# Kernel optimization log

Hardware: AMD Instinct MI355X
Metric: run time of the kernel (lower is better)

Reference implementation:

```python
import jax, jax.numpy as jnp
import numpy as np

N_EMBD = 768
N_HEAD = 12
B, T = 4, 2048
EPS = 1e-5


def layernorm(x, w, b):
    mu = jnp.mean(x, axis=-1, keepdims=True)
    var = jnp.mean(jnp.square(x - mu), axis=-1, keepdims=True)
    return (x - mu) * jax.lax.rsqrt(var + EPS) * w + b


def setup_inputs() -> dict:
    key = jax.random.key(0)
    ks = jax.random.split(key, 6)
    C = N_EMBD
    s = 0.02
    return {
        "x": jax.random.normal(ks[0], (B, T, C), jnp.float32),
        "ln1_w": jnp.ones((C,), jnp.float32),
        "ln1_b": jnp.zeros((C,), jnp.float32),
        "W_qkv": jax.random.normal(ks[1], (C, 3 * C), jnp.float32) * s,
        "b_qkv": jnp.zeros((3 * C,), jnp.float32),
        "W_attnproj": jax.random.normal(ks[2], (C, C), jnp.float32) * s,
        "b_attnproj": jnp.zeros((C,), jnp.float32),
        "ln2_w": jnp.ones((C,), jnp.float32),
        "ln2_b": jnp.zeros((C,), jnp.float32),
        "W_fc": jax.random.normal(ks[3], (C, 4 * C), jnp.float32) * s,
        "b_fc": jnp.zeros((4 * C,), jnp.float32),
        "W_mlpproj": jax.random.normal(ks[4], (4 * C, C), jnp.float32) * s,
        "b_mlpproj": jnp.zeros((C,), jnp.float32),
    }


def reference(x, ln1_w, ln1_b, W_qkv, b_qkv, W_attnproj, b_attnproj,
              ln2_w, ln2_b, W_fc, b_fc, W_mlpproj, b_mlpproj):
    Bx, Tx, C = x.shape
    H = N_HEAD
    Dh = C // H

    # --- attention branch ---
    h = layernorm(x, ln1_w, ln1_b)
    qkv = h @ W_qkv + b_qkv                       # [B, T, 3C]
    q, k, v = jnp.split(qkv, 3, axis=-1)
    q = q.reshape(Bx, Tx, H, Dh).transpose(0, 2, 1, 3)  # [B, H, T, Dh]
    k = k.reshape(Bx, Tx, H, Dh).transpose(0, 2, 1, 3)
    v = v.reshape(Bx, Tx, H, Dh).transpose(0, 2, 1, 3)
    att = jnp.einsum('bhqd,bhkd->bhqk', q, k) * (1.0 / np.sqrt(Dh))
    att = jax.nn.softmax(att, axis=-1)            # full softmax attention (no mask)
    y = jnp.einsum('bhqk,bhkd->bhqd', att, v)     # [B, H, T, Dh]
    y = y.transpose(0, 2, 1, 3).reshape(Bx, Tx, C)
    y = y @ W_attnproj + b_attnproj
    x = x + y

    # --- MLP branch ---
    h = layernorm(x, ln2_w, ln2_b)
    h = jax.nn.gelu(h @ W_fc + b_fc, approximate=False)
    h = h @ W_mlpproj + b_mlpproj
    return x + h
```

## Files before the change

### kernel.cpp

```cpp
#include <hip/hip_runtime.h>

typedef __bf16 bf16x8 __attribute__((ext_vector_type(8)));
typedef __bf16 bf16x4 __attribute__((ext_vector_type(4)));
typedef float f32x4 __attribute__((ext_vector_type(4)));
typedef unsigned short u16;
typedef unsigned long long u64;

#define GL2LDS(gp, lp) __builtin_amdgcn_global_load_lds(                      \
    (const __attribute__((address_space(1))) void*)(gp),                      \
    (__attribute__((address_space(3))) void*)(lp), 16, 0, 0)

__device__ __forceinline__ u16 f2u(float f) {
    __bf16 h = (__bf16)f;
    return __builtin_bit_cast(u16, h);
}

__device__ __forceinline__ float fexp2(float x) {
    float r;
    asm("v_exp_f32 %0, %1" : "=v"(r) : "v"(x));
    return r;
}

__device__ __forceinline__ float frcp(float x) {
    float r;
    asm("v_rcp_f32 %0, %1" : "=v"(r) : "v"(x));
    return r;
}

__device__ __forceinline__ float gelu(float x) {
    const float a = x * x;
    const float b = fmaf(a, 0.10294323f, 2.30220795f);
    const float u = fexp2(x * b);
    const float r = frcp(1.0f + u);
    return (x > 8.0f) ? x : x * u * r;
}

template <int N>
__device__ __forceinline__ void waitv() {
    if constexpr (N == 0) asm volatile("s_waitcnt vmcnt(0)" ::: "memory");
    else if constexpr (N == 3) asm volatile("s_waitcnt vmcnt(3)" ::: "memory");
    else if constexpr (N == 4) asm volatile("s_waitcnt vmcnt(4)" ::: "memory");
    else if constexpr (N == 6) asm volatile("s_waitcnt vmcnt(6)" ::: "memory");
    else if constexpr (N == 8) asm volatile("s_waitcnt vmcnt(8)" ::: "memory");
}

__device__ __forceinline__ f32x4 mfma16(bf16x8 a, bf16x8 b, f32x4 c) {
    return __builtin_amdgcn_mfma_f32_16x16x32_bf16(a, b, c, 0, 0, 0);
}

__global__ __launch_bounds__(256) void transpose_kernel(
    const float* __restrict__ W, u16* __restrict__ Wt, int K, int N) {
    __shared__ float tile[32][33];
    const int tx = threadIdx.x & 31, ty = threadIdx.x >> 5;
    const int n0 = blockIdx.x * 32, k0 = blockIdx.y * 32;
#pragma unroll
    for (int i = 0; i < 4; i++)
        tile[ty + 8 * i][tx] = W[(size_t)(k0 + ty + 8 * i) * N + n0 + tx];
    __syncthreads();
#pragma unroll
    for (int i = 0; i < 4; i++)
        Wt[(size_t)(n0 + ty + 8 * i) * K + k0 + tx] = f2u(tile[tx][ty + 8 * i]);
}

__global__ __launch_bounds__(256) void ln_kernel(
    const float* __restrict__ xin, const float* __restrict__ wgt,
    const float* __restrict__ bia, u16* __restrict__ outp) {
    const int row = blockIdx.x, t = threadIdx.x;
    const float* xr = xin + (size_t)row * 768;
    float v0 = xr[t], v1 = xr[t + 256], v2 = xr[t + 512];
    float s = v0 + v1 + v2;
    float ss = v0 * v0 + v1 * v1 + v2 * v2;
#pragma unroll
    for (int off = 32; off; off >>= 1) {
        s += __shfl_xor(s, off);
        ss += __shfl_xor(ss, off);
    }
    __shared__ float red[8];
    const int w = t >> 6;
    if ((t & 63) == 0) { red[w] = s; red[4 + w] = ss; }
    __syncthreads();
    s  = red[0] + red[1] + red[2] + red[3];
    ss = red[4] + red[5] + red[6] + red[7];
    const float mu = s * (1.f / 768.f);
    const float var = ss * (1.f / 768.f) - mu * mu;
    const float rs = rsqrtf(var + 1e-5f);
    u16* orow = outp + (size_t)row * 768;
    orow[t]       = f2u((v0 - mu) * rs * wgt[t]       + bia[t]);
    orow[t + 256] = f2u((v1 - mu) * rs * wgt[t + 256] + bia[t + 256]);
    orow[t + 512] = f2u((v2 - mu) * rs * wgt[t + 512] + bia[t + 512]);
}

template <int BM, int BN, int DEPTH, int EPI>
__global__ __launch_bounds__(256, 3) void gemm_bt(
    const u16* __restrict__ A, const u16* __restrict__ Bt,
    const float* __restrict__ bias, const float* __restrict__ res,
    void* __restrict__ outp, u16* __restrict__ vt, int M, int N, int K) {
    constexpr int MM = BM / 32;
    constexpr int NN = BN / 32;
    constexpr int L = BM / 64 + BN / 64;
    constexpr int NBUF = DEPTH + 1;
    __shared__ __align__(16) u16 As[NBUF][BM * 32];
    __shared__ __align__(16) u16 Bs[NBUF][BN * 32];
    const int t = threadIdx.x;
    const int lane = t & 63, w = t >> 6;
    const int wg0 = blockIdx.y * gridDim.x + blockIdx.x;
    const int xcd = wg0 & 7, loc = wg0 >> 3;
    const int gx = gridDim.x, gy = gridDim.y;
    const int m0 = (xcd * (gy >> 3) + loc / gx) * BM;
    const int n0 = (loc % gx) * BN;
    const int wm = (w >> 1) * (BM / 2), wn = (w & 1) * (BN / 2);
    const int lq = lane & 15, g = lane >> 4;

    f32x4 acc[MM][NN];
#pragma unroll
    for (int i = 0; i < MM; i++)
#pragma unroll
        for (int j = 0; j < NN; j++) acc[i][j] = (f32x4){0.f, 0.f, 0.f, 0.f};

    const int srow = t >> 2;
    const int scl = (t & 3) ^ ((t >> 3) & 3);
    const u16* gA0 = A + (size_t)(m0 + srow) * K + scl * 8;
    const u16* gA1 = A + (size_t)(m0 + 64 + srow) * K + scl * 8;
    const u16* gB0 = Bt + (size_t)(n0 + srow) * K + scl * 8;
    const u16* gB1 = Bt + (size_t)(n0 + 64 + srow) * K + scl * 8;

    const int cph = g ^ ((lq >> 1) & 3);
    const int KT = K >> 5;

#define STAGE(buf, kt)                                                        \
    do {                                                                      \
        const int k0_ = (kt) << 5;                                            \
        char* lA_ = (char*)As[buf] + w * 1024;                                \
        char* lB_ = (char*)Bs[buf] + w * 1024;                                \
        GL2LDS(gA0 + k0_, lA_);                                               \
        if (BM == 128) GL2LDS(gA1 + k0_, lA_ + 4096);                         \
        GL2LDS(gB0 + k0_, lB_);                                               \
        if (BN == 128) GL2LDS(gB1 + k0_, lB_ + 4096);                         \
    } while (0)

#pragma unroll
    for (int d = 0; d < DEPTH; d++) STAGE(d, d);
    int cur = 0;
    for (int kt = 0; kt < KT; ++kt) {
        const int ahead = KT - 1 - kt;
        if (ahead >= DEPTH - 1) waitv<(DEPTH - 1) * L>();
        else if (DEPTH == 3 && ahead == 1) waitv<L>();
        else waitv<0>();
        __builtin_amdgcn_s_barrier();
        __builtin_amdgcn_sched_barrier(0);
        const char* rA = (char*)As[cur] + (wm + lq) * 64 + cph * 16;
        const char* rB = (char*)Bs[cur] + (wn + lq) * 64 + cph * 16;
        bf16x8 af[MM], bfr[NN];
#pragma unroll
        for (int m = 0; m < MM; m++) af[m] = *(const bf16x8*)(rA + m * 1024);
#pragma unroll
        for (int n = 0; n < NN; n++) bfr[n] = *(const bf16x8*)(rB + n * 1024);
#pragma unroll
        for (int m = 0; m < MM; m++)
#pragma unroll
            for (int n = 0; n < NN; n++)
                acc[m][n] = mfma16(af[m], bfr[n], acc[m][n]);
        if (kt + DEPTH < KT) {
            int nb = cur + DEPTH;
            if (nb >= NBUF) nb -= NBUF;
            STAGE(nb, kt + DEPTH);
        }
        cur = (cur == NBUF - 1) ? 0 : cur + 1;
    }
#undef STAGE

#pragma unroll
    for (int n = 0; n < NN; n++) {
        const int col = n0 + wn + 16 * n + lq;
        const float bv = bias[col];
#pragma unroll
        for (int m = 0; m < MM; m++) {
            const int rbase = m0 + wm + 16 * m + 4 * g;
            if constexpr (EPI == 0) {
                if (col < 1536) {
                    const float sc = (col < 768) ? 0.18033688f : 1.0f;
#pragma unroll
                    for (int r = 0; r < 4; r++) {
                        const size_t idx = (size_t)(rbase + r) * N + col;
                        ((u16*)outp)[idx] = f2u((acc[m][n][r] + bv) * sc);
                    }
                } else {
                    const int d = col - 1536;
                    bf16x4 pk;
#pragma unroll
                    for (int r = 0; r < 4; r++)
                        pk[r] = (__bf16)(acc[m][n][r] + bv);
                    u16* vrow = vt +
                        ((size_t)((rbase >> 11) * 12 + (d >> 6)) * 64 + (d & 63)) * 2048 +
                        (rbase & 2047);
                    *(u64*)vrow = __builtin_bit_cast(u64, pk);
                }
            } else {
#pragma unroll
                for (int r = 0; r < 4; r++) {
                    const size_t idx = (size_t)(rbase + r) * N + col;
                    const float v = acc[m][n][r] + bv;
                    if constexpr (EPI == 1) {
                        ((float*)outp)[idx] = v + res[idx];
                    } else {
                        ((u16*)outp)[idx] = f2u(gelu(v));
                    }
                }
            }
        }
    }
}

__global__ __launch_bounds__(256, 3) void gemm_k64(
    const u16* __restrict__ A, const u16* __restrict__ Bt,
    const float* __restrict__ bias, const float* __restrict__ res,
    float* __restrict__ outp, int M, int N, int K) {
    __shared__ __align__(16) u16 As[2][4096];
    __shared__ __align__(16) u16 Bs[2][8192];
    const int t = threadIdx.x;
    const int lane = t & 63, w = t >> 6;
    const int wg0 = blockIdx.y * gridDim.x + blockIdx.x;
    const int xcd = wg0 & 7, loc = wg0 >> 3;
    const int gx = gridDim.x, gy = gridDim.y;
    const int m0 = (xcd * (gy >> 3) + loc / gx) * 64;
    const int n0 = (loc % gx) * 128;
    const int wm = (w >> 1) * 32, wn = (w & 1) * 64;
    const int lq = lane & 15, g = lane >> 4;

    f32x4 acc[2][4];
#pragma unroll
    for (int i = 0; i < 2; i++)
#pragma unroll
        for (int j = 0; j < 4; j++) acc[i][j] = (f32x4){0.f, 0.f, 0.f, 0.f};

    const int srow8 = w * 8 + (lane >> 3);
    const int scol = ((lane & 7) ^ (lane >> 3)) * 8;
    const u16* gA_0 = A + (size_t)(m0 + srow8) * K + scol;
    const u16* gA_1 = A + (size_t)(m0 + 32 + srow8) * K + scol;
    const u16* gB_0 = Bt + (size_t)(n0 + srow8) * K + scol;
    const u16* gB_1 = Bt + (size_t)(n0 + 32 + srow8) * K + scol;
    const u16* gB_2 = Bt + (size_t)(n0 + 64 + srow8) * K + scol;
    const u16* gB_3 = Bt + (size_t)(n0 + 96 + srow8) * K + scol;

    const int KT = K >> 6;

#define STAGE64(buf, kt)                                                      \
    do {                                                                      \
        const int ko_ = (kt) << 6;                                            \
        GL2LDS(gA_0 + ko_, (char*)As[buf] + w * 1024);                        \
        GL2LDS(gA_1 + ko_, (char*)As[buf] + 4096 + w * 1024);                 \
        GL2LDS(gB_0 + ko_, (char*)Bs[buf] + w * 1024);                        \
        GL2LDS(gB_1 + ko_, (char*)Bs[buf] + 4096 + w * 1024);                 \
        GL2LDS(gB_2 + ko_, (char*)Bs[buf] + 8192 + w * 1024);                 \
        GL2LDS(gB_3 + ko_, (char*)Bs[buf] + 12288 + w * 1024);                \
    } while (0)

    STAGE64(0, 0);
    STAGE64(1, 1);
    for (int kt = 0; kt < KT; ++kt) {
        if (kt + 1 < KT) waitv<6>(); else waitv<0>();
        __builtin_amdgcn_s_barrier();
        __builtin_amdgcn_sched_barrier(0);
        const char* aB = (char*)As[kt & 1] + (wm + lq) * 128;
        const char* bB = (char*)Bs[kt & 1] + (wn + lq) * 128;
        const int sw = lq & 7;
#pragma unroll
        for (int s = 0; s < 2; s++) {
            const int co = (((s << 2) + g) ^ sw) << 4;
            bf16x8 af[2], bfr[4];
#pragma unroll
            for (int m = 0; m < 2; m++)
                af[m] = *(const bf16x8*)(aB + m * 2048 + co);
#pragma unroll
            for (int n = 0; n < 4; n++)
                bfr[n] = *(const bf16x8*)(bB + n * 2048 + co);
            __builtin_amdgcn_s_setprio(1);
#pragma unroll
            for (int m = 0; m < 2; m++)
#pragma unroll
                for (int n = 0; n < 4; n++)
                    acc[m][n] = mfma16(af[m], bfr[n], acc[m][n]);
            __builtin_amdgcn_s_setprio(0);
        }
        __builtin_amdgcn_sched_barrier(0);
        __builtin_amdgcn_s_barrier();
        if (kt + 2 < KT) STAGE64(kt & 1, kt + 2);
    }
#undef STAGE64

#pragma unroll
    for (int n = 0; n < 4; n++) {
        const int col = n0 + wn + 16 * n + lq;
        const float bv = bias[col];
#pragma unroll
        for (int m = 0; m < 2; m++) {
            const int rbase = m0 + wm + 16 * m + 4 * g;
#pragma unroll
            for (int r = 0; r < 4; r++) {
                const size_t idx = (size_t)(rbase + r) * N + col;
                outp[idx] = acc[m][n][r] + bv + res[idx];
            }
        }
    }
}

__global__ __launch_bounds__(256, 3) void attn_kernel(
    const u16* __restrict__ qkv, const u16* __restrict__ Vt,
    u16* __restrict__ y) {
    __shared__ __align__(16) u16 Ks[2][4096];
    __shared__ __align__(16) u16 Vts[2][4096];
    __shared__ __align__(16) u16 Ps[4][2048];
    const int t = threadIdx.x, lane = t & 63, w = t >> 6;
    int wg = blockIdx.y * gridDim.x + blockIdx.x;
    wg = (wg & 7) * ((gridDim.x * gridDim.y) >> 3) + (wg >> 3);
    const int bh = wg / gridDim.x;
    const int b = bh / 12, h = bh % 12;
    const int q0 = (wg % gridDim.x) * 128 + w * 32;
    const int lq = lane & 15, g = lane >> 4;
    const int swz = (lq & 7) << 4;

    bf16x8 qf[2][2];
#pragma unroll
    for (int qh = 0; qh < 2; qh++) {
        const u16* qp =
            qkv + (size_t)(b * 2048 + q0 + qh * 16 + lq) * 2304 + h * 64 + g * 8;
        qf[qh][0] = *(const bf16x8*)(qp);
        qf[qh][1] = *(const bf16x8*)(qp + 32);
    }
    bf16x8 ones;
#pragma unroll
    for (int i = 0; i < 8; i++) ones[i] = (__bf16)1.0f;

    f32x4 acc_o[2][4], acc_s[2];
#pragma unroll
    for (int qh = 0; qh < 2; qh++) {
        acc_s[qh] = (f32x4){0.f, 0.f, 0.f, 0.f};
#pragma unroll
        for (int f = 0; f < 4; f++) acc_o[qh][f] = (f32x4){0.f, 0.f, 0.f, 0.f};
    }

    const int srow = t >> 3, sc = (t & 7) ^ (srow & 7);
    const u16* kg = qkv + 768 + h * 64 + sc * 8 + (size_t)(b * 2048 + srow) * 2304;
    const u16* vg = Vt + (size_t)(bh * 64 + srow) * 2048 + sc * 8;

    int cur = 0;
    GL2LDS(kg, (char*)Ks[0] + w * 1024);
    GL2LDS(kg + (size_t)32 * 2304, (char*)Ks[0] + w * 1024 + 4096);
    GL2LDS(vg, (char*)Vts[0] + w * 1024);
    GL2LDS(vg + 32 * 2048, (char*)Vts[0] + w * 1024 + 4096);
    __syncthreads();

    for (int k0 = 0; k0 < 2048; k0 += 64) {
        if (k0 + 64 < 2048) {
            const int kn = k0 + 64;
            GL2LDS(kg + (size_t)kn * 2304, (char*)Ks[cur ^ 1] + w * 1024);
            GL2LDS(kg + (size_t)(kn + 32) * 2304,
                   (char*)Ks[cur ^ 1] + w * 1024 + 4096);
            GL2LDS(vg + kn, (char*)Vts[cur ^ 1] + w * 1024);
            GL2LDS(vg + 32 * 2048 + kn, (char*)Vts[cur ^ 1] + w * 1024 + 4096);
        }
        const char* KB = (const char*)Ks[cur];
        const char* VB = (const char*)Vts[cur];

        f32x4 st[2][4];
        __builtin_amdgcn_s_setprio(1);
#pragma unroll
        for (int kb = 0; kb < 4; kb++) {
            st[0][kb] = (f32x4){0.f, 0.f, 0.f, 0.f};
            st[1][kb] = (f32x4){0.f, 0.f, 0.f, 0.f};
            const char* kr = KB + (kb * 16 + lq) * 128;
#pragma unroll
            for (int dh = 0; dh < 2; dh++) {
                const bf16x8 kf =
                    *(const bf16x8*)(kr + ((((dh << 2) + g) << 4) ^ swz));
                st[0][kb] = mfma16(kf, qf[0][dh], st[0][kb]);
                st[1][kb] = mfma16(kf, qf[1][dh], st[1][kb]);
            }
        }
        __builtin_amdgcn_s_setprio(0);

#pragma unroll
        for (int qh = 0; qh < 2; qh++) {
            char* pw = (char*)Ps[w] + (qh * 16 + lq) * 128 + ((g & 1) << 3);
#pragma unroll
            for (int kb = 0; kb < 4; kb++) {
                bf16x4 pb;
#pragma unroll
                for (int r = 0; r < 4; r++)
                    pb[r] = (__bf16)fexp2(st[qh][kb][r]);
                *(u64*)(pw + ((((kb << 1) + (g >> 1)) << 4) ^ swz)) =
                    __builtin_bit_cast(u64, pb);
            }
        }

        __builtin_amdgcn_s_setprio(1);
#pragma unroll
        for (int kk = 0; kk < 2; kk++) {
            const int co = ((kk << 2) + g) << 4;
            bf16x8 vf[4];
#pragma unroll
            for (int f = 0; f < 4; f++)
                vf[f] = *(const bf16x8*)(VB + (16 * f + lq) * 128 + (co ^ swz));
#pragma unroll
            for (int qh = 0; qh < 2; qh++) {
                const bf16x8 pf = *(const bf16x8*)(
                    (const char*)Ps[w] + (qh * 16 + lq) * 128 + (co ^ swz));
#pragma unroll
                for (int f = 0; f < 4; f++)
                    acc_o[qh][f] = mfma16(vf[f], pf, acc_o[qh][f]);
                acc_s[qh] = mfma16(ones, pf, acc_s[qh]);
            }
        }
        __builtin_amdgcn_s_setprio(0);
        __syncthreads();
        cur ^= 1;
    }

#pragma unroll
    for (int qh = 0; qh < 2; qh++) {
        const float rinv = frcp(acc_s[qh][0]);
        char* yb = (char*)(y + (size_t)(b * 2048 + q0 + qh * 16 + lq) * 768 +
                           h * 64);
#pragma unroll
        for (int f = 0; f < 4; f++) {
            bf16x4 pk;
#pragma unroll
            for (int r = 0; r < 4; r++) pk[r] = (__bf16)(acc_o[qh][f][r] * rinv);
            *(u64*)(yb + f * 32 + g * 8) = __builtin_bit_cast(u64, pk);
        }
    }
}

extern "C" void kernel_launch(void* const* d_in, const int* in_sizes, int n_in,
                              void* d_out, int out_size, void* d_ws,
                              size_t ws_size, hipStream_t stream) {
    const float* x    = (const float*)d_in[0];
    const float* ln1w = (const float*)d_in[1];
    const float* ln1b = (const float*)d_in[2];
    const float* Wqkv = (const float*)d_in[3];
    const float* bqkv = (const float*)d_in[4];
    const float* Wap  = (const float*)d_in[5];
    const float* bap  = (const float*)d_in[6];
    const float* ln2w = (const float*)d_in[7];
    const float* ln2b = (const float*)d_in[8];
    const float* Wfc  = (const float*)d_in[9];
    const float* bfc  = (const float*)d_in[10];
    const float* Wmp  = (const float*)d_in[11];
    const float* bmp  = (const float*)d_in[12];
    float* out = (float*)d_out;

    char* ws = (char*)d_ws;
    u16* Wt_qkv = (u16*)(ws);
    u16* Wt_ap  = (u16*)(ws + 3538944);
    u16* Wt_fc  = (u16*)(ws + 4718592);
    u16* Wt_mp  = (u16*)(ws + 9437184);
    u16* bufA   = (u16*)(ws + 14155776);
    u16* bufB   = (u16*)(ws + 26738688);
    u16* VtBuf  = (u16*)(ws + 64487424);

    transpose_kernel<<<dim3(72, 24), 256, 0, stream>>>(Wqkv, Wt_qkv, 768, 2304);
    transpose_kernel<<<dim3(24, 24), 256, 0, stream>>>(Wap, Wt_ap, 768, 768);
    transpose_kernel<<<dim3(96, 24), 256, 0, stream>>>(Wfc, Wt_fc, 768, 3072);
    transpose_kernel<<<dim3(24, 96), 256, 0, stream>>>(Wmp, Wt_mp, 3072, 768);

    ln_kernel<<<8192, 256, 0, stream>>>(x, ln1w, ln1b, bufA);
    gemm_bt<128, 128, 2, 0><<<dim3(18, 64), 256, 0, stream>>>(
        bufA, Wt_qkv, bqkv, nullptr, bufB, VtBuf, 8192, 2304, 768);
    attn_kernel<<<dim3(16, 48), 256, 0, stream>>>(bufB, VtBuf, bufA);
    gemm_k64<<<dim3(6, 128), 256, 0, stream>>>(
        bufA, Wt_ap, bap, x, out, 8192, 768, 768);
    ln_kernel<<<8192, 256, 0, stream>>>(out, ln2w, ln2b, bufA);
    gemm_bt<128, 128, 2, 2><<<dim3(24, 64), 256, 0, stream>>>(
        bufA, Wt_fc, bfc, nullptr, bufB, nullptr, 8192, 3072, 768);
    gemm_k64<<<dim3(6, 128), 256, 0, stream>>>(
        bufB, Wt_mp, bmp, out, out, 8192, 768, 3072);
}
```

Measured before the change: 267.1 us.

## Use BK=64 double-buffered GEMM and explicit vmcnt pipelining in attention

The QKV and FC GEMMs go from three 32-wide K-stage buffers to two 64-wide ones, with an XOR swizzle over 8 chunks, setprio around the MFMAs, and a second barrier before refilling the buffer just consumed. Occupancy hint drops from 3 to 2 blocks per CU to fit the larger LDS tiles. The attention kernel now prefetches two K/V tiles ahead with vmcnt waits instead of one tile plus syncthreads. The aim is fewer barriers per K step and better overlap of loads with MFMA, at the cost of more LDS and lower occupancy.

```diff
diff --git a/kernel.cpp b/kernel.cpp
--- a/kernel.cpp
+++ b/kernel.cpp
@@ -38,7 +38,6 @@
 template <int N>
 __device__ __forceinline__ void waitv() {
     if constexpr (N == 0) asm volatile("s_waitcnt vmcnt(0)" ::: "memory");
-    else if constexpr (N == 3) asm volatile("s_waitcnt vmcnt(3)" ::: "memory");
     else if constexpr (N == 4) asm volatile("s_waitcnt vmcnt(4)" ::: "memory");
     else if constexpr (N == 6) asm volatile("s_waitcnt vmcnt(6)" ::: "memory");
     else if constexpr (N == 8) asm volatile("s_waitcnt vmcnt(8)" ::: "memory");
@@ -90,99 +89,97 @@
     orow[t + 512] = f2u((v2 - mu) * rs * wgt[t + 512] + bia[t + 512]);
 }
 
-template <int BM, int BN, int DEPTH, int EPI>
-__global__ __launch_bounds__(256, 3) void gemm_bt(
+template <int EPI>
+__global__ __launch_bounds__(256, 2) void gemm128(
     const u16* __restrict__ A, const u16* __restrict__ Bt,
-    const float* __restrict__ bias, const float* __restrict__ res,
-    void* __restrict__ outp, u16* __restrict__ vt, int M, int N, int K) {
-    constexpr int MM = BM / 32;
-    constexpr int NN = BN / 32;
-    constexpr int L = BM / 64 + BN / 64;
-    constexpr int NBUF = DEPTH + 1;
-    __shared__ __align__(16) u16 As[NBUF][BM * 32];
-    __shared__ __align__(16) u16 Bs[NBUF][BN * 32];
+    const float* __restrict__ bias, void* __restrict__ outp,
+    u16* __restrict__ vt, int M, int N, int K) {
+    __shared__ __align__(16) u16 As[2][8192];
+    __shared__ __align__(16) u16 Bs[2][8192];
     const int t = threadIdx.x;
     const int lane = t & 63, w = t >> 6;
     const int wg0 = blockIdx.y * gridDim.x + blockIdx.x;
     const int xcd = wg0 & 7, loc = wg0 >> 3;
-    const int gx = gridDim.x, gy = gridDim.y;
-    const int m0 = (xcd * (gy >> 3) + loc / gx) * BM;
-    const int n0 = (loc % gx) * BN;
-    const int wm = (w >> 1) * (BM / 2), wn = (w & 1) * (BN / 2);
+    const int gx = gridDim.x;
+    const int m0 = (xcd * 8 + loc / gx) * 128;
+    const int n0 = (loc % gx) * 128;
+    const int wm = (w >> 1) * 64, wn = (w & 1) * 64;
     const int lq = lane & 15, g = lane >> 4;
 
-    f32x4 acc[MM][NN];
-#pragma unroll
-    for (int i = 0; i < MM; i++)
-#pragma unroll
-        for (int j = 0; j < NN; j++) acc[i][j] = (f32x4){0.f, 0.f, 0.f, 0.f};
-
-    const int srow = t >> 2;
-    const int scl = (t & 3) ^ ((t >> 3) & 3);
-    const u16* gA0 = A + (size_t)(m0 + srow) * K + scl * 8;
-    const u16* gA1 = A + (size_t)(m0 + 64 + srow) * K + scl * 8;
-    const u16* gB0 = Bt + (size_t)(n0 + srow) * K + scl * 8;
-    const u16* gB1 = Bt + (size_t)(n0 + 64 + srow) * K + scl * 8;
-
-    const int cph = g ^ ((lq >> 1) & 3);
-    const int KT = K >> 5;
-
-#define STAGE(buf, kt)                                                        \
+    f32x4 acc[4][4];
+#pragma unroll
+    for (int i = 0; i < 4; i++)
+#pragma unroll
+        for (int j = 0; j < 4; j++) acc[i][j] = (f32x4){0.f, 0.f, 0.f, 0.f};
+
+    const int srow8 = w * 8 + (lane >> 3);
+    const int scol = ((lane & 7) ^ (lane >> 3)) * 8;
+    const u16* gA_[4];
+    const u16* gB_[4];
+#pragma unroll
+    for (int a = 0; a < 4; a++) {
+        gA_[a] = A + (size_t)(m0 + a * 32 + srow8) * K + scol;
+        gB_[a] = Bt + (size_t)(n0 + a * 32 + srow8) * K + scol;
+    }
+    const int KT = K >> 6;
+
+#define STAGE128(buf, kt)                                                     \
     do {                                                                      \
-        const int k0_ = (kt) << 5;                                            \
-        char* lA_ = (char*)As[buf] + w * 1024;                                \
-        char* lB_ = (char*)Bs[buf] + w * 1024;                                \
-        GL2LDS(gA0 + k0_, lA_);                                               \
-        if (BM == 128) GL2LDS(gA1 + k0_, lA_ + 4096);                         \
-        GL2LDS(gB0 + k0_, lB_);                                               \
-        if (BN == 128) GL2LDS(gB1 + k0_, lB_ + 4096);                         \
+        const int ko_ = (kt) << 6;                                            \
+        _Pragma("unroll")                                                     \
+        for (int a = 0; a < 4; a++) {                                         \
+            GL2LDS(gA_[a] + ko_, (char*)As[buf] + a * 4096 + w * 1024);       \
+            GL2LDS(gB_[a] + ko_, (char*)Bs[buf] + a * 4096 + w * 1024);       \
+        }                                                                     \
     } while (0)
 
-#pragma unroll
-    for (int d = 0; d < DEPTH; d++) STAGE(d, d);
-    int cur = 0;
+    STAGE128(0, 0);
+    STAGE128(1, 1);
     for (int kt = 0; kt < KT; ++kt) {
-        const int ahead = KT - 1 - kt;
-        if (ahead >= DEPTH - 1) waitv<(DEPTH - 1) * L>();
-        else if (DEPTH == 3 && ahead == 1) waitv<L>();
-        else waitv<0>();
-        __builtin_amdgcn_s_barrier();
-        __builtin_amdgcn_sched_barrier(0);
-        const char* rA = (char*)As[cur] + (wm + lq) * 64 + cph * 16;
-        const char* rB = (char*)Bs[cur] + (wn + lq) * 64 + cph * 16;
-        bf16x8 af[MM], bfr[NN];
-#pragma unroll
-        for (int m = 0; m < MM; m++) af[m] = *(const bf16x8*)(rA + m * 1024);
-#pragma unroll
-        for (int n = 0; n < NN; n++) bfr[n] = *(const bf16x8*)(rB + n * 1024);
-#pragma unroll
-        for (int m = 0; m < MM; m++)
-#pragma unroll
-            for (int n = 0; n < NN; n++)
-                acc[m][n] = mfma16(af[m], bfr[n], acc[m][n]);
-        if (kt + DEPTH < KT) {
-            int nb = cur + DEPTH;
-            if (nb >= NBUF) nb -= NBUF;
-            STAGE(nb, kt + DEPTH);
-        }
-        cur = (cur == NBUF - 1) ? 0 : cur + 1;
-    }
-#undef STAGE
-
-#pragma unroll
-    for (int n = 0; n < NN; n++) {
+        if (kt + 1 < KT) waitv<8>(); else waitv<0>();
+        __builtin_amdgcn_s_barrier();
+        __builtin_amdgcn_sched_barrier(0);
+        const char* aB = (char*)As[kt & 1] + (wm + lq) * 128;
+        const char* bB = (char*)Bs[kt & 1] + (wn + lq) * 128;
+        const int sw = lq & 7;
+#pragma unroll
+        for (int s = 0; s < 2; s++) {
+            const int co = (((s << 2) + g) ^ sw) << 4;
+            bf16x8 af[4], bfr[4];
+#pragma unroll
+            for (int m = 0; m < 4; m++)
+                af[m] = *(const bf16x8*)(aB + m * 2048 + co);
+#pragma unroll
+            for (int n = 0; n < 4; n++)
+                bfr[n] = *(const bf16x8*)(bB + n * 2048 + co);
+            __builtin_amdgcn_s_setprio(1);
+#pragma unroll
+            for (int m = 0; m < 4; m++)
+#pragma unroll
+                for (int n = 0; n < 4; n++)
+                    acc[m][n] = mfma16(af[m], bfr[n], acc[m][n]);
+            __builtin_amdgcn_s_setprio(0);
+        }
+        __builtin_amdgcn_sched_barrier(0);
+        __builtin_amdgcn_s_barrier();
+        if (kt + 2 < KT) STAGE128(kt & 1, kt + 2);
+    }
+#undef STAGE128
+
+#pragma unroll
+    for (int n = 0; n < 4; n++) {
         const int col = n0 + wn + 16 * n + lq;
         const float bv = bias[col];
 #pragma unroll
-        for (int m = 0; m < MM; m++) {
+        for (int m = 0; m < 4; m++) {
             const int rbase = m0 + wm + 16 * m + 4 * g;
             if constexpr (EPI == 0) {
                 if (col < 1536) {
-                    const float sc = (col < 768) ? 0.18033688f : 1.0f;
+                    const float qs = (col < 768) ? 0.18033688f : 1.0f;
 #pragma unroll
                     for (int r = 0; r < 4; r++) {
                         const size_t idx = (size_t)(rbase + r) * N + col;
-                        ((u16*)outp)[idx] = f2u((acc[m][n][r] + bv) * sc);
+                        ((u16*)outp)[idx] = f2u((acc[m][n][r] + bv) * qs);
                     }
                 } else {
                     const int d = col - 1536;
@@ -199,12 +196,7 @@
 #pragma unroll
                 for (int r = 0; r < 4; r++) {
                     const size_t idx = (size_t)(rbase + r) * N + col;
-                    const float v = acc[m][n][r] + bv;
-                    if constexpr (EPI == 1) {
-                        ((float*)outp)[idx] = v + res[idx];
-                    } else {
-                        ((u16*)outp)[idx] = f2u(gelu(v));
-                    }
+                    ((u16*)outp)[idx] = f2u(gelu(acc[m][n][r] + bv));
                 }
             }
         }
@@ -343,24 +335,25 @@
     const u16* kg = qkv + 768 + h * 64 + sc * 8 + (size_t)(b * 2048 + srow) * 2304;
     const u16* vg = Vt + (size_t)(bh * 64 + srow) * 2048 + sc * 8;
 
-    int cur = 0;
-    GL2LDS(kg, (char*)Ks[0] + w * 1024);
-    GL2LDS(kg + (size_t)32 * 2304, (char*)Ks[0] + w * 1024 + 4096);
-    GL2LDS(vg, (char*)Vts[0] + w * 1024);
-    GL2LDS(vg + 32 * 2048, (char*)Vts[0] + w * 1024 + 4096);
-    __syncthreads();
-
-    for (int k0 = 0; k0 < 2048; k0 += 64) {
-        if (k0 + 64 < 2048) {
-            const int kn = k0 + 64;
-            GL2LDS(kg + (size_t)kn * 2304, (char*)Ks[cur ^ 1] + w * 1024);
-            GL2LDS(kg + (size_t)(kn + 32) * 2304,
-                   (char*)Ks[cur ^ 1] + w * 1024 + 4096);
-            GL2LDS(vg + kn, (char*)Vts[cur ^ 1] + w * 1024);
-            GL2LDS(vg + 32 * 2048 + kn, (char*)Vts[cur ^ 1] + w * 1024 + 4096);
-        }
-        const char* KB = (const char*)Ks[cur];
-        const char* VB = (const char*)Vts[cur];
+#define STAGEKV(buf, kt)                                                      \
+    do {                                                                      \
+        const int kn_ = (kt) * 64;                                            \
+        GL2LDS(kg + (size_t)kn_ * 2304, (char*)Ks[buf] + w * 1024);           \
+        GL2LDS(kg + (size_t)(kn_ + 32) * 2304,                                \
+               (char*)Ks[buf] + w * 1024 + 4096);                             \
+        GL2LDS(vg + kn_, (char*)Vts[buf] + w * 1024);                         \
+        GL2LDS(vg + 32 * 2048 + kn_, (char*)Vts[buf] + w * 1024 + 4096);      \
+    } while (0)
+
+    STAGEKV(0, 0);
+    STAGEKV(1, 1);
+    for (int kt = 0; kt < 32; ++kt) {
+        const int buf = kt & 1;
+        if (kt + 1 < 32) waitv<4>(); else waitv<0>();
+        __builtin_amdgcn_s_barrier();
+        __builtin_amdgcn_sched_barrier(0);
+        const char* KB = (const char*)Ks[buf];
+        const char* VB = (const char*)Vts[buf];
 
         f32x4 st[2][4];
         __builtin_amdgcn_s_setprio(1);
@@ -412,9 +405,11 @@
             }
         }
         __builtin_amdgcn_s_setprio(0);
-        __syncthreads();
-        cur ^= 1;
-    }
+        __builtin_amdgcn_sched_barrier(0);
+        __builtin_amdgcn_s_barrier();
+        if (kt + 2 < 32) STAGEKV(buf, kt + 2);
+    }
+#undef STAGEKV
 
 #pragma unroll
     for (int qh = 0; qh < 2; qh++) {
@@ -422,7 +417,7 @@
         char* yb = (char*)(y + (size_t)(b * 2048 + q0 + qh * 16 + lq) * 768 +
                            h * 64);
 #pragma unroll
-        for (int f = 0; f < 4; f++) {
+    for (int f = 0; f < 4; f++) {
             bf16x4 pk;
 #pragma unroll
             for (int r = 0; r < 4; r++) pk[r] = (__bf16)(acc_o[qh][f][r] * rinv);
@@ -464,14 +459,14 @@
     transpose_kernel<<<dim3(24, 96), 256, 0, stream>>>(Wmp, Wt_mp, 3072, 768);
 
     ln_kernel<<<8192, 256, 0, stream>>>(x, ln1w, ln1b, bufA);
-    gemm_bt<128, 128, 2, 0><<<dim3(18, 64), 256, 0, stream>>>(
-        bufA, Wt_qkv, bqkv, nullptr, bufB, VtBuf, 8192, 2304, 768);
+    gemm128<0><<<dim3(18, 64), 256, 0, stream>>>(
+        bufA, Wt_qkv, bqkv, bufB, VtBuf, 8192, 2304, 768);
     attn_kernel<<<dim3(16, 48), 256, 0, stream>>>(bufB, VtBuf, bufA);
     gemm_k64<<<dim3(6, 128), 256, 0, stream>>>(
         bufA, Wt_ap, bap, x, out, 8192, 768, 768);
     ln_kernel<<<8192, 256, 0, stream>>>(out, ln2w, ln2b, bufA);
-    gemm_bt<128, 128, 2, 2><<<dim3(24, 64), 256, 0, stream>>>(
-        bufA, Wt_fc, bfc, nullptr, bufB, nullptr, 8192, 3072, 768);
+    gemm128<2><<<dim3(24, 64), 256, 0, stream>>>(
+        bufA, Wt_fc, bfc, bufB, nullptr, 8192, 3072, 768);
     gemm_k64<<<dim3(6, 128), 256, 0, stream>>>(
         bufB, Wt_mp, bmp, out, out, 8192, 768, 3072);
 }
```

Result: no change. 269.9 us (+1.1%).
